# Kernel optimization log

Hardware: AMD Instinct MI355X
Metric: run time of the kernel (lower is better)

The kernel has to match this reference:

```python
import jax, jax.numpy as jnp
import numpy as np

IN_F = 4096
OUT_F = 11008
P8 = 128
P6 = 256
P4 = IN_F - P8 - P6  # 3712


def setup_inputs() -> dict:
    key = jax.random.key(0)
    k1, k2, k3, k4 = jax.random.split(key, 4)
    x = jax.random.normal(k1, (32, 8, IN_F), dtype=jnp.float32)
    W = jax.random.normal(k2, (OUT_F, IN_F), dtype=jnp.float32) * 0.02
    bias = jax.random.normal(k3, (OUT_F,), dtype=jnp.float32) * 0.01
    # channel permutation: first P4 channels -> 4-bit, next P6 -> 6-bit, last P8 -> 8-bit outliers
    reorder_index = jax.random.permutation(k4, IN_F).astype(jnp.int32)
    return {"x": x, "W": W, "bias": bias, "reorder_index": reorder_index}


def _quant(v, bits):
    # symmetric per-row quantization (per-token for acts, per-out-channel for weights)
    qmax = float(2 ** (bits - 1) - 1)
    s = jnp.max(jnp.abs(v), axis=-1, keepdims=True) / qmax
    s = jnp.where(s == 0, jnp.ones_like(s), s)
    q = jnp.round(jnp.clip(v / s, -qmax, qmax))
    return q, s


def reference(x, W, bias, reorder_index):
    bsz, q_len, F = x.shape
    xr = x.reshape(bsz * q_len, F)[:, reorder_index]  # reorder_quantize_x gather
    Wr = W[:, reorder_index]                          # reorder_quantize_w4 gather
    y = jnp.zeros((bsz * q_len, W.shape[0]), dtype=x.dtype)
    start = 0
    for bits, n in ((4, P4), (6, P6), (8, P8)):
        qa, sa = _quant(xr[:, start:start + n], bits)      # [T,n], [T,1]
        qb, sb = _quant(Wr[:, start:start + n], bits)      # [O,n], [O,1]
        # dequantized partial matmul: (qa @ qb.T) * sa * sb.T
        y = y + jnp.einsum('tn,on->to', qa, qb) * (sa * sb.T)
        start += n
    y = y + bias
    return y.reshape(bsz, q_len, -1)
```

## Files before the change

kernel.cpp:

```cpp
#include <hip/hip_runtime.h>
#include <stdint.h>

#define T_ROWS 256
#define KF 4096
#define OF 11008

typedef int   v4i __attribute__((ext_vector_type(4)));
typedef float v4f __attribute__((ext_vector_type(4)));

typedef const __attribute__((address_space(1))) uint8_t* gptr_t;
typedef __attribute__((address_space(3))) uint8_t* lptr_t;

__global__ __launch_bounds__(256) void perm_k(const int* __restrict__ idx,
                                              int* __restrict__ src_of) {
    __shared__ uint8_t g[KF];
    __shared__ int cnt[3][256];
    __shared__ int exc[3][256];
    const int t = threadIdx.x;
    for (int i = 0; i < 16; ++i) {
        int p = t * 16 + i;
        int seg = p < 3712 ? 0 : (p < 3968 ? 1 : 2);
        g[idx[p]] = (uint8_t)seg;
    }
    __syncthreads();
    int c0 = 0, c1 = 0, c2 = 0;
    for (int i = 0; i < 16; ++i) {
        int s = g[t * 16 + i];
        c0 += (s == 0); c1 += (s == 1); c2 += (s == 2);
    }
    cnt[0][t] = c0; cnt[1][t] = c1; cnt[2][t] = c2;
    __syncthreads();
    if (t < 192) {
        int s = t >> 6, l = t & 63;
        int run = 0;
        for (int j = 0; j < 4; ++j) {
            int x = cnt[s][j * 64 + l];
            int inc = x;
#pragma unroll
            for (int off = 1; off < 64; off <<= 1) {
                int y = __shfl_up(inc, off);
                if (l >= off) inc += y;
            }
            exc[s][j * 64 + l] = run + inc - x;
            run += __shfl(inc, 63);
        }
    }
    __syncthreads();
    int off0 = exc[0][t], off1 = 3712 + exc[1][t], off2 = 3968 + exc[2][t];
    for (int i = 0; i < 16; ++i) {
        int c = t * 16 + i;
        int s = g[c];
        int d = (s == 0) ? off0++ : (s == 1) ? off1++ : off2++;
        src_of[d] = c;
    }
}

__global__ __launch_bounds__(256) void quant_k(const float* __restrict__ x,
                                               const float* __restrict__ W,
                                               const int* __restrict__ src_of,
                                               int8_t* __restrict__ qX,
                                               int8_t* __restrict__ qW,
                                               float* __restrict__ sX,
                                               float* __restrict__ sW) {
    __shared__ float rowbuf[KF];
    __shared__ float lmax[256];
    __shared__ float sm[3];
    const int b = blockIdx.x;
    const int t = threadIdx.x;
    const int w = t >> 6, ln = t & 63;
    const float* src; int8_t* qout; float* scales; int r; int nrows;
    if (b < T_ROWS) { src = x; qout = qX; scales = sX; r = b; nrows = T_ROWS; }
    else           { src = W; qout = qW; scales = sW; r = b - T_ROWS; nrows = OF; }
    const float* row = src + (size_t)r * KF;

#pragma unroll
    for (int j = 0; j < 4; ++j) {
        const uint8_t* srcp = (const uint8_t*)(row + j * 1024 + t * 4);
        __builtin_amdgcn_global_load_lds((gptr_t)srcp, (lptr_t)&rowbuf[j * 1024 + w * 256], 16, 0, 0);
    }

    const int seg = t < 232 ? 0 : (t < 248 ? 1 : 2);
    const float qmax = seg == 0 ? 7.f : (seg == 1 ? 31.f : 127.f);
    int c[16];
#pragma unroll
    for (int i = 0; i < 4; ++i) {
        v4i ci = *(const v4i*)&src_of[t * 16 + i * 4];
        c[i*4+0] = ci[0]; c[i*4+1] = ci[1]; c[i*4+2] = ci[2]; c[i*4+3] = ci[3];
    }
    __syncthreads();

    float v[16];
    float mx = 0.f;
#pragma unroll
    for (int i = 0; i < 16; ++i) { v[i] = rowbuf[c[i]]; mx = fmaxf(mx, fabsf(v[i])); }
    lmax[t] = mx;
    __syncthreads();
    if (w == 0) {
        float m = fmaxf(fmaxf(lmax[ln], lmax[ln + 64]), lmax[ln + 128]);
        if (ln < 40) m = fmaxf(m, lmax[ln + 192]);
#pragma unroll
        for (int off = 32; off; off >>= 1) m = fmaxf(m, __shfl_xor(m, off));
        if (ln == 0) sm[0] = m;
    } else if (w == 1) {
        float m = ln < 16 ? lmax[232 + ln] : 0.f;
#pragma unroll
        for (int off = 8; off; off >>= 1) m = fmaxf(m, __shfl_xor(m, off));
        if (ln == 0) sm[1] = m;
    } else if (w == 2) {
        float m = ln < 8 ? lmax[248 + ln] : 0.f;
#pragma unroll
        for (int off = 4; off; off >>= 1) m = fmaxf(m, __shfl_xor(m, off));
        if (ln == 0) sm[2] = m;
    }
    __syncthreads();
    float s = sm[seg] / qmax;
    if (s == 0.f) s = 1.f;
    if (t == 0 || t == 232 || t == 248) scales[seg * nrows + r] = s;
    const float rs = 1.0f / s;
    union { int8_t bb[16]; v4i q; } u;
#pragma unroll
    for (int i = 0; i < 16; ++i) {
        float qv = rintf(fminf(fmaxf(v[i] * rs, -qmax), qmax));
        u.bb[i] = (int8_t)qv;
    }
    *(v4i*)(qout + (size_t)r * KF + t * 16) = u.q;
}

__global__ __launch_bounds__(256, 2)
void gemm_k(const int8_t* __restrict__ qX, const int8_t* __restrict__ qW,
            const float* __restrict__ sX, const float* __restrict__ sW,
            const float* __restrict__ bias, float* __restrict__ out) {
    __shared__ __align__(16) int8_t lB[3][64 * 128];

    const int bid = blockIdx.x;
    const int swz = (bid & 7) * 43 + (bid >> 3);
    const int row0 = (swz & 1) * 128;
    const int col0 = (swz >> 1) * 64;
    const int tid = threadIdx.x;
    const int lane = tid & 63;
    const int w = tid >> 6;
    const int lr = lane >> 3, lc = lane & 7;
    const int kg = lane >> 4;
    const int cr = lane & 15;

    v4i iacc[2][4];
    v4f facc[2][4];
#pragma unroll
    for (int m = 0; m < 2; ++m)
#pragma unroll
        for (int n = 0; n < 4; ++n) {
            iacc[m][n][0]=0; iacc[m][n][1]=0; iacc[m][n][2]=0; iacc[m][n][3]=0;
            facc[m][n][0]=0.f; facc[m][n][1]=0.f; facc[m][n][2]=0.f; facc[m][n][3]=0.f;
        }

    const int8_t* aRow[2];
    aRow[0] = qX + (size_t)(row0 + w * 32 + cr) * KF;
    aRow[1] = qX + (size_t)(row0 + w * 32 + 16 + cr) * KF;

    auto stageB = [&](int slot, int step) {
        const int k0 = step * 128;
        const int sc = (lc ^ lr) << 4;
#pragma unroll
        for (int j = 0; j < 2; ++j) {
            const int brow = j * 32 + w * 8;
            const uint8_t* src = (const uint8_t*)qW + (size_t)(col0 + brow + lr) * KF + k0 + sc;
            __builtin_amdgcn_global_load_lds((gptr_t)src, (lptr_t)&lB[slot][brow * 128], 16, 0, 0);
        }
    };

    auto loadA = [&](v4i (&a)[2][2], int step) {
        const int kb = step * 128 + kg * 16;
#pragma unroll
        for (int m = 0; m < 2; ++m)
#pragma unroll
            for (int kk = 0; kk < 2; ++kk) {
                const int8_t* p = aRow[m] + kb + kk * 64;
                asm volatile("global_load_dwordx4 %0, %1, off"
                             : "=v"(a[m][kk]) : "v"(p) : "memory");
            }
    };

    auto flush = [&](int seg) {
#pragma unroll
        for (int m = 0; m < 2; ++m) {
            float sa[4];
#pragma unroll
            for (int rr = 0; rr < 4; ++rr)
                sa[rr] = sX[seg * T_ROWS + row0 + w * 32 + m * 16 + ((lane >> 4) << 2) + rr];
#pragma unroll
            for (int n = 0; n < 4; ++n) {
                const float sb = sW[seg * OF + col0 + n * 16 + (lane & 15)];
#pragma unroll
                for (int rr = 0; rr < 4; ++rr) {
                    facc[m][n][rr] += (float)iacc[m][n][rr] * (sa[rr] * sb);
                    iacc[m][n][rr] = 0;
                }
            }
        }
    };

    auto body = [&](int t, v4i (&aCur)[2][2], v4i (&aNext)[2][2]) {
        __builtin_amdgcn_s_barrier();
        v4i bf[4][2];
        const int8_t* pb = &lB[t % 3][0];
#pragma unroll
        for (int n = 0; n < 4; ++n) {
            const int brow = n * 16 + cr;
#pragma unroll
            for (int kk = 0; kk < 2; ++kk) {
                const int ch = (kk * 4 + kg) ^ (brow & 7);
                bf[n][kk] = *(const v4i*)(pb + brow * 128 + ch * 16);
            }
        }
        if (t + 2 < 32) stageB((t + 2) % 3, t + 2);
        if (t + 1 < 32) loadA(aNext, t + 1);
        if (t < 30)       asm volatile("s_waitcnt vmcnt(6) lgkmcnt(0)" ::: "memory");
        else if (t == 30) asm volatile("s_waitcnt vmcnt(4) lgkmcnt(0)" ::: "memory");
        else              asm volatile("s_waitcnt vmcnt(0) lgkmcnt(0)" ::: "memory");
        __builtin_amdgcn_sched_barrier(0);
#pragma unroll
        for (int kk = 0; kk < 2; ++kk)
#pragma unroll
            for (int m = 0; m < 2; ++m)
#pragma unroll
                for (int n = 0; n < 4; ++n)
                    iacc[m][n] = __builtin_amdgcn_mfma_i32_16x16x64_i8(aCur[m][kk], bf[n][kk], iacc[m][n], 0, 0, 0);
        if (t == 28) flush(0);
        else if (t == 30) flush(1);
    };

    v4i aA[2][2], aB[2][2];
    stageB(0, 0);
    stageB(1, 1);
    loadA(aA, 0);
    asm volatile("s_waitcnt vmcnt(6)" ::: "memory");

    for (int tt = 0; tt < 32; tt += 2) {
        body(tt,     aA, aB);
        body(tt + 1, aB, aA);
    }
    flush(2);

#pragma unroll
    for (int m = 0; m < 2; ++m)
#pragma unroll
        for (int n = 0; n < 4; ++n) {
            const int colg = col0 + n * 16 + (lane & 15);
            const float bv = bias[colg];
#pragma unroll
            for (int rr = 0; rr < 4; ++rr) {
                const int rowg = row0 + w * 32 + m * 16 + ((lane >> 4) << 2) + rr;
                out[(size_t)rowg * OF + colg] = facc[m][n][rr] + bv;
            }
        }
}

extern "C" void kernel_launch(void* const* d_in, const int* in_sizes, int n_in,
                              void* d_out, int out_size, void* d_ws, size_t ws_size,
                              hipStream_t stream) {
    const float* x    = (const float*)d_in[0];
    const float* W    = (const float*)d_in[1];
    const float* bias = (const float*)d_in[2];
    const int*   ridx = (const int*)d_in[3];
    float* out = (float*)d_out;

    uint8_t* ws = (uint8_t*)d_ws;
    int8_t* qX = (int8_t*)ws;
    int8_t* qW = (int8_t*)(ws + 1048576);
    float*  sX = (float*)(ws + 46137344);
    float*  sW = (float*)(ws + 46140416);
    int* src_of = (int*)(ws + 46272512);

    perm_k<<<1, 256, 0, stream>>>(ridx, src_of);
    quant_k<<<T_ROWS + OF, 256, 0, stream>>>(x, W, src_of, qX, qW, sX, sW);
    gemm_k<<<344, 256, 0, stream>>>(qX, qW, sX, sW, bias, out);
}
```

Baseline: 79.10 us.

## Scatter quantized bytes via destination map instead of gathering floats in LDS

```diff
diff --git a/kernel.cpp b/kernel.cpp
--- a/kernel.cpp
+++ b/kernel.cpp
@@ -12,7 +12,7 @@
 typedef __attribute__((address_space(3))) uint8_t* lptr_t;
 
 __global__ __launch_bounds__(256) void perm_k(const int* __restrict__ idx,
-                                              int* __restrict__ src_of) {
+                                              unsigned short* __restrict__ dest_of) {
     __shared__ uint8_t g[KF];
     __shared__ int cnt[3][256];
     __shared__ int exc[3][256];
@@ -51,79 +51,82 @@
         int c = t * 16 + i;
         int s = g[c];
         int d = (s == 0) ? off0++ : (s == 1) ? off1++ : off2++;
-        src_of[d] = c;
+        dest_of[c] = (unsigned short)d;
     }
 }
 
 __global__ __launch_bounds__(256) void quant_k(const float* __restrict__ x,
                                                const float* __restrict__ W,
-                                               const int* __restrict__ src_of,
+                                               const unsigned short* __restrict__ dest_of,
                                                int8_t* __restrict__ qX,
                                                int8_t* __restrict__ qW,
                                                float* __restrict__ sX,
                                                float* __restrict__ sW) {
-    __shared__ float rowbuf[KF];
-    __shared__ float lmax[256];
-    __shared__ float sm[3];
+    __shared__ uint8_t qlds[KF];
+    __shared__ float smw[3][4];
     const int b = blockIdx.x;
     const int t = threadIdx.x;
     const int w = t >> 6, ln = t & 63;
-    const float* src; int8_t* qout; float* scales; int r; int nrows;
-    if (b < T_ROWS) { src = x; qout = qX; scales = sX; r = b; nrows = T_ROWS; }
-    else           { src = W; qout = qW; scales = sW; r = b - T_ROWS; nrows = OF; }
-    const float* row = src + (size_t)r * KF;
-
-#pragma unroll
-    for (int j = 0; j < 4; ++j) {
-        const uint8_t* srcp = (const uint8_t*)(row + j * 1024 + t * 4);
-        __builtin_amdgcn_global_load_lds((gptr_t)srcp, (lptr_t)&rowbuf[j * 1024 + w * 256], 16, 0, 0);
-    }
-
-    const int seg = t < 232 ? 0 : (t < 248 ? 1 : 2);
-    const float qmax = seg == 0 ? 7.f : (seg == 1 ? 31.f : 127.f);
-    int c[16];
+    const bool isX = b < T_ROWS;
+    const int r = isX ? b : b - T_ROWS;
+    const float* row = (isX ? x : W) + (size_t)r * KF;
+    int8_t* qout = isX ? qX : qW;
+    float* scales = isX ? sX : sW;
+    const int nrows = isX ? T_ROWS : OF;
+
+    v4f v[4];
+    unsigned short d16[16];
 #pragma unroll
     for (int i = 0; i < 4; ++i) {
-        v4i ci = *(const v4i*)&src_of[t * 16 + i * 4];
-        c[i*4+0] = ci[0]; c[i*4+1] = ci[1]; c[i*4+2] = ci[2]; c[i*4+3] = ci[3];
-    }
-    __syncthreads();
-
-    float v[16];
-    float mx = 0.f;
-#pragma unroll
-    for (int i = 0; i < 16; ++i) { v[i] = rowbuf[c[i]]; mx = fmaxf(mx, fabsf(v[i])); }
-    lmax[t] = mx;
-    __syncthreads();
-    if (w == 0) {
-        float m = fmaxf(fmaxf(lmax[ln], lmax[ln + 64]), lmax[ln + 128]);
-        if (ln < 40) m = fmaxf(m, lmax[ln + 192]);
-#pragma unroll
-        for (int off = 32; off; off >>= 1) m = fmaxf(m, __shfl_xor(m, off));
-        if (ln == 0) sm[0] = m;
-    } else if (w == 1) {
-        float m = ln < 16 ? lmax[232 + ln] : 0.f;
-#pragma unroll
-        for (int off = 8; off; off >>= 1) m = fmaxf(m, __shfl_xor(m, off));
-        if (ln == 0) sm[1] = m;
-    } else if (w == 2) {
-        float m = ln < 8 ? lmax[248 + ln] : 0.f;
-#pragma unroll
-        for (int off = 4; off; off >>= 1) m = fmaxf(m, __shfl_xor(m, off));
-        if (ln == 0) sm[2] = m;
-    }
-    __syncthreads();
-    float s = sm[seg] / qmax;
-    if (s == 0.f) s = 1.f;
-    if (t == 0 || t == 232 || t == 248) scales[seg * nrows + r] = s;
-    const float rs = 1.0f / s;
-    union { int8_t bb[16]; v4i q; } u;
-#pragma unroll
-    for (int i = 0; i < 16; ++i) {
-        float qv = rintf(fminf(fmaxf(v[i] * rs, -qmax), qmax));
-        u.bb[i] = (int8_t)qv;
-    }
-    *(v4i*)(qout + (size_t)r * KF + t * 16) = u.q;
+        v[i] = *(const v4f*)(row + i * 1024 + t * 4);
+        *(ushort4*)&d16[i * 4] = *(const ushort4*)(dest_of + i * 1024 + t * 4);
+    }
+
+    float m0 = 0.f, m1 = 0.f, m2 = 0.f;
+#pragma unroll
+    for (int i = 0; i < 4; ++i)
+#pragma unroll
+        for (int j = 0; j < 4; ++j) {
+            const int d = d16[i * 4 + j];
+            const float a = fabsf(v[i][j]);
+            m0 = (d < 3712)              ? fmaxf(m0, a) : m0;
+            m1 = (d >= 3712 && d < 3968) ? fmaxf(m1, a) : m1;
+            m2 = (d >= 3968)             ? fmaxf(m2, a) : m2;
+        }
+#pragma unroll
+    for (int off = 32; off; off >>= 1) {
+        m0 = fmaxf(m0, __shfl_xor(m0, off));
+        m1 = fmaxf(m1, __shfl_xor(m1, off));
+        m2 = fmaxf(m2, __shfl_xor(m2, off));
+    }
+    if (ln == 0) { smw[0][w] = m0; smw[1][w] = m1; smw[2][w] = m2; }
+    __syncthreads();
+    m0 = fmaxf(fmaxf(smw[0][0], smw[0][1]), fmaxf(smw[0][2], smw[0][3]));
+    m1 = fmaxf(fmaxf(smw[1][0], smw[1][1]), fmaxf(smw[1][2], smw[1][3]));
+    m2 = fmaxf(fmaxf(smw[2][0], smw[2][1]), fmaxf(smw[2][2], smw[2][3]));
+    float s0 = m0 / 7.f;   if (s0 == 0.f) s0 = 1.f;
+    float s1 = m1 / 31.f;  if (s1 == 0.f) s1 = 1.f;
+    float s2 = m2 / 127.f; if (s2 == 0.f) s2 = 1.f;
+    if (t == 0) {
+        scales[r] = s0;
+        scales[nrows + r] = s1;
+        scales[2 * nrows + r] = s2;
+    }
+    const float r0 = 1.f / s0, r1 = 1.f / s1, r2 = 1.f / s2;
+
+#pragma unroll
+    for (int i = 0; i < 4; ++i)
+#pragma unroll
+        for (int j = 0; j < 4; ++j) {
+            const int d = d16[i * 4 + j];
+            const float qmax = (d < 3712) ? 7.f : ((d < 3968) ? 31.f : 127.f);
+            const float rs   = (d < 3712) ? r0  : ((d < 3968) ? r1  : r2);
+            const float qv = rintf(fminf(fmaxf(v[i][j] * rs, -qmax), qmax));
+            qlds[d] = (uint8_t)(int8_t)(int)qv;
+        }
+    __syncthreads();
+    const v4i q = *(const v4i*)&qlds[t * 16];
+    *(v4i*)(qout + (size_t)r * KF + t * 16) = q;
 }
 
 __global__ __launch_bounds__(256, 2)
@@ -269,9 +272,9 @@
     int8_t* qW = (int8_t*)(ws + 1048576);
     float*  sX = (float*)(ws + 46137344);
     float*  sW = (float*)(ws + 46140416);
-    int* src_of = (int*)(ws + 46272512);
-
-    perm_k<<<1, 256, 0, stream>>>(ridx, src_of);
-    quant_k<<<T_ROWS + OF, 256, 0, stream>>>(x, W, src_of, qX, qW, sX, sW);
+    unsigned short* dest_of = (unsigned short*)(ws + 46272512);
+
+    perm_k<<<1, 256, 0, stream>>>(ridx, dest_of);
+    quant_k<<<T_ROWS + OF, 256, 0, stream>>>(x, W, dest_of, qX, qW, sX, sW);
     gemm_k<<<344, 256, 0, stream>>>(qX, qW, sX, sW, bias, out);
 }
```

After: 95.42 us. 20.6% more time.

## Process four rows per quant block with double-buffered async LDS loads

Applied to the files above, without the earlier changes.

```diff
diff --git a/kernel.cpp b/kernel.cpp
--- a/kernel.cpp
+++ b/kernel.cpp
@@ -62,68 +62,85 @@
                                                int8_t* __restrict__ qW,
                                                float* __restrict__ sX,
                                                float* __restrict__ sW) {
-    __shared__ float rowbuf[KF];
+    __shared__ float rowbuf[2][KF];
     __shared__ float lmax[256];
     __shared__ float sm[3];
-    const int b = blockIdx.x;
+    const int bx = blockIdx.x;
     const int t = threadIdx.x;
     const int w = t >> 6, ln = t & 63;
-    const float* src; int8_t* qout; float* scales; int r; int nrows;
-    if (b < T_ROWS) { src = x; qout = qX; scales = sX; r = b; nrows = T_ROWS; }
-    else           { src = W; qout = qW; scales = sW; r = b - T_ROWS; nrows = OF; }
-    const float* row = src + (size_t)r * KF;
-
-#pragma unroll
-    for (int j = 0; j < 4; ++j) {
-        const uint8_t* srcp = (const uint8_t*)(row + j * 1024 + t * 4);
-        __builtin_amdgcn_global_load_lds((gptr_t)srcp, (lptr_t)&rowbuf[j * 1024 + w * 256], 16, 0, 0);
-    }
+    const bool isX = bx < 64;
+    const int r0 = (isX ? bx : bx - 64) * 4;
+    const float* base = isX ? x : W;
+    int8_t* qout = isX ? qX : qW;
+    float* scales = isX ? sX : sW;
+    const int nrows = isX ? T_ROWS : OF;
 
     const int seg = t < 232 ? 0 : (t < 248 ? 1 : 2);
     const float qmax = seg == 0 ? 7.f : (seg == 1 ? 31.f : 127.f);
+
     int c[16];
 #pragma unroll
     for (int i = 0; i < 4; ++i) {
         v4i ci = *(const v4i*)&src_of[t * 16 + i * 4];
         c[i*4+0] = ci[0]; c[i*4+1] = ci[1]; c[i*4+2] = ci[2]; c[i*4+3] = ci[3];
     }
-    __syncthreads();
-
-    float v[16];
-    float mx = 0.f;
-#pragma unroll
-    for (int i = 0; i < 16; ++i) { v[i] = rowbuf[c[i]]; mx = fmaxf(mx, fabsf(v[i])); }
-    lmax[t] = mx;
-    __syncthreads();
-    if (w == 0) {
-        float m = fmaxf(fmaxf(lmax[ln], lmax[ln + 64]), lmax[ln + 128]);
-        if (ln < 40) m = fmaxf(m, lmax[ln + 192]);
-#pragma unroll
-        for (int off = 32; off; off >>= 1) m = fmaxf(m, __shfl_xor(m, off));
-        if (ln == 0) sm[0] = m;
-    } else if (w == 1) {
-        float m = ln < 16 ? lmax[232 + ln] : 0.f;
-#pragma unroll
-        for (int off = 8; off; off >>= 1) m = fmaxf(m, __shfl_xor(m, off));
-        if (ln == 0) sm[1] = m;
-    } else if (w == 2) {
-        float m = ln < 8 ? lmax[248 + ln] : 0.f;
-#pragma unroll
-        for (int off = 4; off; off >>= 1) m = fmaxf(m, __shfl_xor(m, off));
-        if (ln == 0) sm[2] = m;
-    }
-    __syncthreads();
-    float s = sm[seg] / qmax;
-    if (s == 0.f) s = 1.f;
-    if (t == 0 || t == 232 || t == 248) scales[seg * nrows + r] = s;
-    const float rs = 1.0f / s;
-    union { int8_t bb[16]; v4i q; } u;
-#pragma unroll
-    for (int i = 0; i < 16; ++i) {
-        float qv = rintf(fminf(fmaxf(v[i] * rs, -qmax), qmax));
-        u.bb[i] = (int8_t)qv;
-    }
-    *(v4i*)(qout + (size_t)r * KF + t * 16) = u.q;
+
+    auto stage = [&](int buf, int rr) {
+        const float* row = base + (size_t)(r0 + rr) * KF;
+#pragma unroll
+        for (int j = 0; j < 4; ++j) {
+            const uint8_t* srcp = (const uint8_t*)(row + j * 1024 + t * 4);
+            __builtin_amdgcn_global_load_lds((gptr_t)srcp,
+                (lptr_t)&rowbuf[buf][j * 1024 + w * 256], 16, 0, 0);
+        }
+    };
+
+    stage(0, 0);
+    for (int r = 0; r < 4; ++r) {
+        if (r < 3) {
+            stage((r + 1) & 1, r + 1);
+            asm volatile("s_waitcnt vmcnt(4)" ::: "memory");
+        } else {
+            asm volatile("s_waitcnt vmcnt(0)" ::: "memory");
+        }
+        __syncthreads();
+        const float* rb = rowbuf[r & 1];
+        float v[16];
+        float mx = 0.f;
+#pragma unroll
+        for (int i = 0; i < 16; ++i) { v[i] = rb[c[i]]; mx = fmaxf(mx, fabsf(v[i])); }
+        lmax[t] = mx;
+        __syncthreads();
+        if (w == 0) {
+            float m = fmaxf(fmaxf(lmax[ln], lmax[ln + 64]), lmax[ln + 128]);
+            if (ln < 40) m = fmaxf(m, lmax[ln + 192]);
+#pragma unroll
+            for (int off = 32; off; off >>= 1) m = fmaxf(m, __shfl_xor(m, off));
+            if (ln == 0) sm[0] = m;
+        } else if (w == 1) {
+            float m = ln < 16 ? lmax[232 + ln] : 0.f;
+#pragma unroll
+            for (int off = 8; off; off >>= 1) m = fmaxf(m, __shfl_xor(m, off));
+            if (ln == 0) sm[1] = m;
+        } else if (w == 2) {
+            float m = ln < 8 ? lmax[248 + ln] : 0.f;
+#pragma unroll
+            for (int off = 4; off; off >>= 1) m = fmaxf(m, __shfl_xor(m, off));
+            if (ln == 0) sm[2] = m;
+        }
+        __syncthreads();
+        float s = sm[seg] / qmax;
+        if (s == 0.f) s = 1.f;
+        if (t == 0 || t == 232 || t == 248) scales[seg * nrows + r0 + r] = s;
+        const float rs = 1.0f / s;
+        union { int8_t bb[16]; v4i q; } u;
+#pragma unroll
+        for (int i = 0; i < 16; ++i) {
+            float qv = rintf(fminf(fmaxf(v[i] * rs, -qmax), qmax));
+            u.bb[i] = (int8_t)qv;
+        }
+        *(v4i*)(qout + (size_t)(r0 + r) * KF + t * 16) = u.q;
+    }
 }
 
 __global__ __launch_bounds__(256, 2)
@@ -272,6 +289,6 @@
     int* src_of = (int*)(ws + 46272512);
 
     perm_k<<<1, 256, 0, stream>>>(ridx, src_of);
-    quant_k<<<T_ROWS + OF, 256, 0, stream>>>(x, W, src_of, qX, qW, sX, sW);
+    quant_k<<<64 + 2752, 256, 0, stream>>>(x, W, src_of, qX, qW, sX, sW);
     gemm_k<<<344, 256, 0, stream>>>(qX, qW, sX, sW, bias, out);
 }
```

Result: slower. 83.03 us (+5.0%).
